# Performance work log

Measured on AMD Instinct MI355X. Metric: run time of the kernel, lower is better.

The kernel has to match this reference:

```python
import jax, jax.numpy as jnp
import numpy as np

N = 100000      # nodes
E = 1600000     # edges (avg degree 16)
IN_DIM = 64
OUT_DIM = 128
BN_EPS = 1e-5


def setup_inputs() -> dict:
    key = jax.random.key(0)
    kx, ke, kw, kb, ks = jax.random.split(key, 5)
    x = jax.random.normal(kx, (N, IN_DIM), dtype=jnp.float32)
    edge_index = jax.random.randint(ke, (2, E), 0, N, dtype=jnp.int32)
    # GCNConv linear weight (no bias inside lin; conv bias separate)
    W = jax.random.normal(kw, (IN_DIM, OUT_DIM), dtype=jnp.float32) / np.sqrt(IN_DIM)
    bias = jax.random.normal(kb, (OUT_DIM,), dtype=jnp.float32) * 0.01
    # skip projection Linear(in_dim, out_dim, bias=False)
    skip_W = jax.random.normal(ks, (IN_DIM, OUT_DIM), dtype=jnp.float32) / np.sqrt(IN_DIM)
    # BatchNorm1d affine params (training-mode batch stats used in forward)
    gamma = jnp.ones((OUT_DIM,), dtype=jnp.float32)
    beta = jnp.zeros((OUT_DIM,), dtype=jnp.float32)
    return {"x": x, "edge_index": edge_index, "W": W, "bias": bias,
            "skip_W": skip_W, "gamma": gamma, "beta": beta}


def _gcn_forward(x, edge_index, W, bias, skip_W, gamma, beta):
    n = x.shape[0]
    # GCNConv, normalize=True, add_self_loops=True (PyG defaults)
    row, col = edge_index[0], edge_index[1]
    loop = jnp.arange(n, dtype=edge_index.dtype)
    row_f = jnp.concatenate([row, loop])   # source nodes
    col_f = jnp.concatenate([col, loop])   # target nodes

    xt = x @ W                             # [N, OUT]
    deg = jax.ops.segment_sum(jnp.ones_like(col_f, dtype=xt.dtype), col_f,
                              num_segments=n)          # >= 1 due to self loops
    dinv = jax.lax.rsqrt(deg)
    norm = dinv[row_f] * dinv[col_f]                    # [E+N]
    msgs = xt[row_f] * norm[:, None]                    # gather + scale
    out = jax.ops.segment_sum(msgs, col_f, num_segments=n) + bias

    # skip-sum (in_dim != out_dim -> project)
    out = out + x @ skip_W

    # BatchNorm1d (training-mode batch statistics), affine
    mean = out.mean(axis=0)
    var = out.var(axis=0)
    out = (out - mean) * jax.lax.rsqrt(var + BN_EPS) * gamma + beta

    # ReLU; dropout p=0.0 -> identity
    return jax.nn.relu(out)


def reference(x, edge_index, W, bias, skip_W, gamma, beta):
    return _gcn_forward(x, edge_index, W, bias, skip_W, gamma, beta)
```

## Files before the change

### kernel.cpp

```cpp
#include <hip/hip_runtime.h>


typedef unsigned short ushort;
typedef __bf16 bf16x8 __attribute__((ext_vector_type(8)));
typedef float f32x4 __attribute__((ext_vector_type(4)));

constexpr int N_NODES = 100000;
constexpr int N_PAD   = 100096;
constexpr int E_EDGES = 1600000;

constexpr int BUCK_SHIFT = 7;
constexpr int NBUCK   = (N_NODES + 127) / 128;
constexpr int NBUCK_P = 784;
constexpr int CHUNK   = 4096;
constexpr int NCHUNK  = (E_EDGES + CHUNK - 1) / CHUNK;
constexpr int SORT_CAP = 4096;

constexpr size_t OFF_SCALE  = 0;
constexpr size_t OFF_DINV   = 256;
constexpr size_t OFF_ROWPTR = 100352;
constexpr size_t OFF_BASE   = 200480;
constexpr size_t OFF_GHIST  = 201280;
constexpr size_t OFF_PART   = OFF_GHIST;
constexpr size_t OFF_BINNED = 507824;
constexpr size_t OFF_XB     = 2107824;
constexpr size_t OFF_U      = 5310896;
constexpr size_t OFF_PRE    = 8513968;
constexpr size_t OFF_XD     = OFF_PRE;
constexpr size_t OFF_BT     = 14920112;

static __device__ __forceinline__ ushort f2bf(float f) {
    union { float f; unsigned u; } v; v.f = f;
    unsigned r = v.u + 0x7FFFu + ((v.u >> 16) & 1u);
    return (ushort)(r >> 16);
}
static __device__ __forceinline__ float bf2f(ushort u) {
    union { unsigned u; float f; } v; v.u = (unsigned)u << 16;
    return v.f;
}

__global__ void k_prep(const float* __restrict__ W, const float* __restrict__ skipW,
                       ushort* __restrict__ Bt) {
    int t = blockIdx.x * 256 + threadIdx.x;
    if (t >= 128 * 128) return;
    int k = t >> 7, n = t & 127;
    float v = (k < 64) ? W[k * 128 + n] : skipW[(k - 64) * 128 + n];
    Bt[n * 128 + k] = f2bf(v);
}

__global__ __launch_bounds__(256) void k_hist(const int* __restrict__ col,
                                              int* __restrict__ gh) {
    __shared__ int h[NBUCK_P];
    int c = blockIdx.x, t = threadIdx.x;
    for (int b = t; b < NBUCK_P; b += 256) h[b] = 0;
    __syncthreads();
    int e0 = c * CHUNK;
#pragma unroll
    for (int i = 0; i < CHUNK / 256; ++i) {
        int e = e0 + i * 256 + t;
        if (e < E_EDGES) atomicAdd(&h[col[e] >> BUCK_SHIFT], 1);
    }
    __syncthreads();
    for (int b = t; b < NBUCK_P; b += 256) gh[c * NBUCK_P + b] = h[b];
}

__global__ __launch_bounds__(512) void k_scan_buckets(int* __restrict__ gh,
                                                      int* __restrict__ base) {
    __shared__ int lds[512];
    int b = blockIdx.x, t = threadIdx.x;
    int v = (t < NCHUNK) ? gh[t * NBUCK_P + b] : 0;
    lds[t] = v;
    __syncthreads();
    int val = v;
#pragma unroll
    for (int off = 1; off < 512; off <<= 1) {
        int add = (t >= off) ? lds[t - off] : 0;
        __syncthreads();
        val += add;
        lds[t] = val;
        __syncthreads();
    }
    if (t < NCHUNK) gh[t * NBUCK_P + b] = val - v;
    if (t == 511) base[b] = val;
}

__global__ __launch_bounds__(1024) void k_scan_bases(int* __restrict__ base,
                                                     int* __restrict__ rowptr) {
    __shared__ int lds[1024];
    int t = threadIdx.x;
    int v = (t < NBUCK) ? base[t] : 0;
    lds[t] = v;
    __syncthreads();
    int val = v;
#pragma unroll
    for (int off = 1; off < 1024; off <<= 1) {
        int add = (t >= off) ? lds[t - off] : 0;
        __syncthreads();
        val += add;
        lds[t] = val;
        __syncthreads();
    }
    if (t < NBUCK) base[t] = val - v;
    if (t == 1023) {
        base[NBUCK] = val;
        rowptr[N_NODES] = val;
    }
}

__global__ __launch_bounds__(256) void k_scatter_bin(const int* __restrict__ row,
                                                     const int* __restrict__ col,
                                                     const int* __restrict__ gh,
                                                     const int* __restrict__ base,
                                                     unsigned int* __restrict__ binned) {
    __shared__ int cur[NBUCK_P];
    int c = blockIdx.x, t = threadIdx.x;
    for (int b = t; b < NBUCK_P; b += 256) {
        int bb = (b < NBUCK) ? base[b] : 0;
        cur[b] = bb + gh[c * NBUCK_P + b];
    }
    __syncthreads();
    int e0 = c * CHUNK;
#pragma unroll
    for (int i = 0; i < CHUNK / 256; ++i) {
        int e = e0 + i * 256 + t;
        if (e < E_EDGES) {
            int d = col[e];
            int s = row[e];
            int p = atomicAdd(&cur[d >> BUCK_SHIFT], 1);
            binned[p] = ((unsigned int)(d & 127) << 17) | (unsigned int)s;
        }
    }
}

__global__ __launch_bounds__(256) void k_sortbucket(unsigned int* __restrict__ binned,
                                                    const int* __restrict__ base,
                                                    int* __restrict__ rowptr,
                                                    float* __restrict__ dinv) {
    __shared__ unsigned int ebuf[SORT_CAP];
    __shared__ int sbuf[SORT_CAP];
    __shared__ int lcnt[128];
    __shared__ int scanb[128];
    __shared__ int lptr[128];
    int b = blockIdx.x, t = threadIdx.x;
    int i0 = base[b], i1 = base[b + 1];
    int cnt = i1 - i0;
    if (cnt > SORT_CAP) cnt = SORT_CAP;
    int n0 = b << BUCK_SHIFT;
    int nn = min(128, N_NODES - n0);

    for (int k = t; k < cnt; k += 256) ebuf[k] = binned[i0 + k];
    if (t < 128) lcnt[t] = 0;
    __syncthreads();
    for (int k = t; k < cnt; k += 256) atomicAdd(&lcnt[ebuf[k] >> 17], 1);
    __syncthreads();

    int myc = (t < 128) ? lcnt[t] : 0;
    if (t < 128) scanb[t] = myc;
    __syncthreads();
    int val = myc;
#pragma unroll
    for (int off = 1; off < 128; off <<= 1) {
        int add = (t < 128 && t >= off) ? scanb[t - off] : 0;
        __syncthreads();
        if (t < 128) {
            val += add;
            scanb[t] = val;
        }
        __syncthreads();
    }
    if (t < 128) {
        int excl = val - myc;
        lptr[t] = excl;
        if (t < nn) {
            rowptr[n0 + t] = i0 + excl;
            dinv[n0 + t] = rsqrtf((float)myc + 1.0f);
        }
    }
    __syncthreads();
    for (int k = t; k < cnt; k += 256) {
        unsigned int e = ebuf[k];
        int j = (int)(e >> 17);
        int p = atomicAdd(&lptr[j], 1);
        sbuf[p] = (int)(e & 0x1FFFF);
    }
    __syncthreads();
    for (int k = t; k < cnt; k += 256) binned[i0 + k] = (unsigned int)sbuf[k];
}

__global__ void k_cast_scale(const float* __restrict__ x, const float* __restrict__ dinv,
                             ushort* __restrict__ xb, ushort* __restrict__ xd) {
    int t = blockIdx.x * blockDim.x + threadIdx.x;
    if (t >= N_PAD * 16) return;
    int c = t >> 4;
    ushort4 b = {0, 0, 0, 0};
    ushort4 o = {0, 0, 0, 0};
    if (c < N_NODES) {
        float d = dinv[c];
        float4 v = ((const float4*)x)[t];
        b.x = f2bf(v.x); b.y = f2bf(v.y); b.z = f2bf(v.z); b.w = f2bf(v.w);
        o.x = f2bf(v.x * d); o.y = f2bf(v.y * d);
        o.z = f2bf(v.z * d); o.w = f2bf(v.w * d);
    }
    ((ushort4*)xb)[t] = b;
    ((ushort4*)xd)[t] = o;
}

__global__ __launch_bounds__(256) void k_agg(const ushort* __restrict__ xd,
                                             const float* __restrict__ dinv,
                                             const int* __restrict__ rowptr,
                                             const unsigned int* __restrict__ csr,
                                             ushort* __restrict__ u) {
    int t = blockIdx.x * blockDim.x + threadIdx.x;
    if (t >= N_PAD * 16) return;
    int c = t >> 4;
    int q = t & 15;
    if (c >= N_NODES) {
        ushort4 z = {0, 0, 0, 0};
        ((ushort4*)u)[t] = z;
        return;
    }
    float dc = dinv[c];
    ushort4 xv = ((const ushort4*)xd)[t];
    float4 acc;
    acc.x = bf2f(xv.x); acc.y = bf2f(xv.y);
    acc.z = bf2f(xv.z); acc.w = bf2f(xv.w);
    int i0 = rowptr[c], i1 = rowptr[c + 1];
    int i = i0;
    for (; i + 4 <= i1; i += 4) {
        int s0 = (int)csr[i];
        int s1 = (int)csr[i + 1];
        int s2 = (int)csr[i + 2];
        int s3 = (int)csr[i + 3];
        ushort4 v0 = ((const ushort4*)xd)[s0 * 16 + q];
        ushort4 v1 = ((const ushort4*)xd)[s1 * 16 + q];
        ushort4 v2 = ((const ushort4*)xd)[s2 * 16 + q];
        ushort4 v3 = ((const ushort4*)xd)[s3 * 16 + q];
        acc.x += bf2f(v0.x) + bf2f(v1.x) + bf2f(v2.x) + bf2f(v3.x);
        acc.y += bf2f(v0.y) + bf2f(v1.y) + bf2f(v2.y) + bf2f(v3.y);
        acc.z += bf2f(v0.z) + bf2f(v1.z) + bf2f(v2.z) + bf2f(v3.z);
        acc.w += bf2f(v0.w) + bf2f(v1.w) + bf2f(v2.w) + bf2f(v3.w);
    }
    for (; i < i1; ++i) {
        int s = (int)csr[i];
        ushort4 v = ((const ushort4*)xd)[s * 16 + q];
        acc.x += bf2f(v.x); acc.y += bf2f(v.y);
        acc.z += bf2f(v.z); acc.w += bf2f(v.w);
    }
    ushort4 o;
    o.x = f2bf(acc.x * dc); o.y = f2bf(acc.y * dc);
    o.z = f2bf(acc.z * dc); o.w = f2bf(acc.w * dc);
    ((ushort4*)u)[t] = o;
}

__global__ __launch_bounds__(256) void k_gemm(const ushort* __restrict__ u,
                                              const ushort* __restrict__ xb,
                                              const ushort* __restrict__ Bt,
                                              const float* __restrict__ bias,
                                              ushort* __restrict__ pre,
                                              float* __restrict__ partial) {
    __shared__ float sred[128];
    __shared__ float qred[128];
    int tid = threadIdx.x;
    int wave = tid >> 6, lane = tid & 63;
    int wm = wave >> 1, wn = wave & 1;
    int l15 = lane & 15, quad = lane >> 4;
    int row0 = blockIdx.x * 128 + wm * 64;
    int col0 = wn * 64;

    if (tid < 128) { sred[tid] = 0.f; qred[tid] = 0.f; }
    __syncthreads();

    bf16x8 af[4][4], bf_[4][4];
#pragma unroll
    for (int kc = 0; kc < 4; ++kc) {
        const ushort* abase = (kc < 2) ? u : xb;
        int ko = (kc & 1) * 32 + quad * 8;
#pragma unroll
        for (int im = 0; im < 4; ++im)
            af[kc][im] = *(const bf16x8*)&abase[(size_t)(row0 + im * 16 + l15) * 64 + ko];
#pragma unroll
        for (int jn = 0; jn < 4; ++jn)
            bf_[kc][jn] = *(const bf16x8*)&Bt[(size_t)(col0 + jn * 16 + l15) * 128 + kc * 32 + quad * 8];
    }

    f32x4 acc[4][4];
#pragma unroll
    for (int a = 0; a < 4; ++a)
#pragma unroll
        for (int b = 0; b < 4; ++b) acc[a][b] = (f32x4){0.f, 0.f, 0.f, 0.f};

#pragma unroll
    for (int kc = 0; kc < 4; ++kc)
#pragma unroll
        for (int im = 0; im < 4; ++im)
#pragma unroll
            for (int jn = 0; jn < 4; ++jn)
                acc[im][jn] = __builtin_amdgcn_mfma_f32_16x16x32_bf16(
                    af[kc][im], bf_[kc][jn], acc[im][jn], 0, 0, 0);

    int coln[4];
    float bi[4];
#pragma unroll
    for (int jn = 0; jn < 4; ++jn) {
        coln[jn] = col0 + jn * 16 + l15;
        bi[jn] = bias[coln[jn]];
    }
    float lsum[4] = {0.f, 0.f, 0.f, 0.f};
    float lsq[4]  = {0.f, 0.f, 0.f, 0.f};
#pragma unroll
    for (int im = 0; im < 4; ++im) {
        int rbase = row0 + im * 16 + quad * 4;
#pragma unroll
        for (int r = 0; r < 4; ++r) {
            int rowi = rbase + r;
            if (rowi < N_NODES) {
#pragma unroll
                for (int jn = 0; jn < 4; ++jn) {
                    float v = acc[im][jn][r] + bi[jn];
                    pre[(size_t)rowi * 128 + coln[jn]] = f2bf(v);
                    lsum[jn] += v;
                    lsq[jn]  += v * v;
                }
            }
        }
    }
#pragma unroll
    for (int jn = 0; jn < 4; ++jn) {
        atomicAdd(&sred[coln[jn]], lsum[jn]);
        atomicAdd(&qred[coln[jn]], lsq[jn]);
    }
    __syncthreads();
    if (tid < 128) {
        partial[(size_t)blockIdx.x * 256 + tid]       = sred[tid];
        partial[(size_t)blockIdx.x * 256 + 128 + tid] = qred[tid];
    }
}

__global__ __launch_bounds__(256) void k_reduce(const float* __restrict__ partial,
                                                const float* __restrict__ gamma,
                                                const float* __restrict__ beta,
                                                float* __restrict__ scaleshift) {
    __shared__ float ls[256], lq[256];
    int j = blockIdx.x;
    int t = threadIdx.x;
    float s = 0.f, q = 0.f;
    for (int p = t; p < NBUCK; p += 256) {
        s += partial[(size_t)p * 256 + j];
        q += partial[(size_t)p * 256 + 128 + j];
    }
    ls[t] = s; lq[t] = q;
    __syncthreads();
#pragma unroll
    for (int off = 128; off > 0; off >>= 1) {
        if (t < off) { ls[t] += ls[t + off]; lq[t] += lq[t + off]; }
        __syncthreads();
    }
    if (t == 0) {
        float mean = ls[0] * (1.0f / N_NODES);
        float var  = lq[0] * (1.0f / N_NODES) - mean * mean;
        float sc   = gamma[j] * rsqrtf(var + 1e-5f);
        scaleshift[j]       = sc;
        scaleshift[128 + j] = beta[j] - mean * sc;
    }
}

__global__ void k_apply(const ushort* __restrict__ pre, float* __restrict__ out,
                        const float* __restrict__ scaleshift) {
    int t = blockIdx.x * blockDim.x + threadIdx.x;
    if (t >= N_NODES * 32) return;
    int j4 = t & 31;
    ushort4 p = ((const ushort4*)pre)[t];
    float4 sc = ((const float4*)scaleshift)[j4];
    float4 sh = ((const float4*)(scaleshift + 128))[j4];
    float4 v;
    v.x = fmaxf(fmaf(bf2f(p.x), sc.x, sh.x), 0.f);
    v.y = fmaxf(fmaf(bf2f(p.y), sc.y, sh.y), 0.f);
    v.z = fmaxf(fmaf(bf2f(p.z), sc.z, sh.z), 0.f);
    v.w = fmaxf(fmaf(bf2f(p.w), sc.w, sh.w), 0.f);
    ((float4*)out)[t] = v;
}

extern "C" void kernel_launch(void* const* d_in, const int* in_sizes, int n_in,
                              void* d_out, int out_size, void* d_ws, size_t ws_size,
                              hipStream_t stream) {
    const float* x      = (const float*)d_in[0];
    const int*   eidx   = (const int*)d_in[1];
    const float* W      = (const float*)d_in[2];
    const float* bias   = (const float*)d_in[3];
    const float* skipW  = (const float*)d_in[4];
    const float* gamma  = (const float*)d_in[5];
    const float* beta   = (const float*)d_in[6];
    float* out = (float*)d_out;
    float* ws  = (float*)d_ws;

    const int* row = eidx;
    const int* col = eidx + E_EDGES;

    float* scaleshift = ws + OFF_SCALE;
    float* dinv       = ws + OFF_DINV;
    int*   rowptr     = (int*)(ws + OFF_ROWPTR);
    int*   base       = (int*)(ws + OFF_BASE);
    int*   gh         = (int*)(ws + OFF_GHIST);
    float* partial    = ws + OFF_PART;
    unsigned int* binned = (unsigned int*)(ws + OFF_BINNED);
    ushort* xb        = (ushort*)(ws + OFF_XB);
    ushort* u         = (ushort*)(ws + OFF_U);
    ushort* xd        = (ushort*)(ws + OFF_XD);
    ushort* pre       = (ushort*)(ws + OFF_PRE);
    ushort* Bt        = (ushort*)(ws + OFF_BT);

    k_prep<<<64, 256, 0, stream>>>(W, skipW, Bt);
    k_hist<<<NCHUNK, 256, 0, stream>>>(col, gh);
    k_scan_buckets<<<NBUCK, 512, 0, stream>>>(gh, base);
    k_scan_bases<<<1, 1024, 0, stream>>>(base, rowptr);
    k_scatter_bin<<<NCHUNK, 256, 0, stream>>>(row, col, gh, base, binned);
    k_sortbucket<<<NBUCK, 256, 0, stream>>>(binned, base, rowptr, dinv);
    k_cast_scale<<<(N_PAD * 16 + 255) / 256, 256, 0, stream>>>(x, dinv, xb, xd);
    k_agg<<<(N_PAD * 16 + 255) / 256, 256, 0, stream>>>(xd, dinv, rowptr, binned, u);
    k_gemm<<<NBUCK, 256, 0, stream>>>(u, xb, Bt, bias, pre, partial);
    k_reduce<<<128, 256, 0, stream>>>(partial, gamma, beta, scaleshift);
    k_apply<<<(N_NODES * 32 + 255) / 256, 256, 0, stream>>>(pre, out, scaleshift);
}
```

Measured before the change: 241.8 us.

## Store scaled features as FP8, fuse cast into sort kernel, unroll gather by 8

The degree-scaled feature copy used by the aggregation gather is now stored as FP8 (4 bytes per 4 features) instead of bf16, halving gather traffic. The separate cast/scale kernel is folded into the per-bucket sort kernel, using its shared dinv values, which removes a launch and one pass over x. The aggregation loop is unrolled to 8 neighbors for more loads in flight. FP8 quantization of messages lowers accuracy and may break tolerance.

```diff
diff --git a/kernel.cpp b/kernel.cpp
--- a/kernel.cpp
+++ b/kernel.cpp
@@ -4,6 +4,7 @@
 typedef unsigned short ushort;
 typedef __bf16 bf16x8 __attribute__((ext_vector_type(8)));
 typedef float f32x4 __attribute__((ext_vector_type(4)));
+typedef float f32x2 __attribute__((ext_vector_type(2)));
 
 constexpr int N_NODES = 100000;
 constexpr int N_PAD   = 100096;
@@ -26,7 +27,7 @@
 constexpr size_t OFF_XB     = 2107824;
 constexpr size_t OFF_U      = 5310896;
 constexpr size_t OFF_PRE    = 8513968;
-constexpr size_t OFF_XD     = OFF_PRE;
+constexpr size_t OFF_XD8    = OFF_PRE;
 constexpr size_t OFF_BT     = 14920112;
 
 static __device__ __forceinline__ ushort f2bf(float f) {
@@ -37,6 +38,12 @@
 static __device__ __forceinline__ float bf2f(ushort u) {
     union { unsigned u; float f; } v; v.u = (unsigned)u << 16;
     return v.f;
+}
+static __device__ __forceinline__ unsigned pack_fp8x4(float a, float b, float c, float d) {
+    int r = 0;
+    r = __builtin_amdgcn_cvt_pk_fp8_f32(a, b, r, false);
+    r = __builtin_amdgcn_cvt_pk_fp8_f32(c, d, r, true);
+    return (unsigned)r;
 }
 
 __global__ void k_prep(const float* __restrict__ W, const float* __restrict__ skipW,
@@ -135,12 +142,16 @@
 __global__ __launch_bounds__(256) void k_sortbucket(unsigned int* __restrict__ binned,
                                                     const int* __restrict__ base,
                                                     int* __restrict__ rowptr,
-                                                    float* __restrict__ dinv) {
+                                                    float* __restrict__ dinv,
+                                                    const float* __restrict__ x,
+                                                    ushort* __restrict__ xb,
+                                                    unsigned* __restrict__ xd8) {
     __shared__ unsigned int ebuf[SORT_CAP];
     __shared__ int sbuf[SORT_CAP];
     __shared__ int lcnt[128];
     __shared__ int scanb[128];
     __shared__ int lptr[128];
+    __shared__ float ldinv[128];
     int b = blockIdx.x, t = threadIdx.x;
     int i0 = base[b], i1 = base[b + 1];
     int cnt = i1 - i0;
@@ -171,9 +182,11 @@
     if (t < 128) {
         int excl = val - myc;
         lptr[t] = excl;
+        float dv = rsqrtf((float)myc + 1.0f);
+        ldinv[t] = dv;
         if (t < nn) {
             rowptr[n0 + t] = i0 + excl;
-            dinv[n0 + t] = rsqrtf((float)myc + 1.0f);
+            dinv[n0 + t] = dv;
         }
     }
     __syncthreads();
@@ -185,27 +198,26 @@
     }
     __syncthreads();
     for (int k = t; k < cnt; k += 256) binned[i0 + k] = (unsigned int)sbuf[k];
-}
-
-__global__ void k_cast_scale(const float* __restrict__ x, const float* __restrict__ dinv,
-                             ushort* __restrict__ xb, ushort* __restrict__ xd) {
-    int t = blockIdx.x * blockDim.x + threadIdx.x;
-    if (t >= N_PAD * 16) return;
-    int c = t >> 4;
-    ushort4 b = {0, 0, 0, 0};
-    ushort4 o = {0, 0, 0, 0};
-    if (c < N_NODES) {
-        float d = dinv[c];
-        float4 v = ((const float4*)x)[t];
-        b.x = f2bf(v.x); b.y = f2bf(v.y); b.z = f2bf(v.z); b.w = f2bf(v.w);
-        o.x = f2bf(v.x * d); o.y = f2bf(v.y * d);
-        o.z = f2bf(v.z * d); o.w = f2bf(v.w * d);
-    }
-    ((ushort4*)xb)[t] = b;
-    ((ushort4*)xd)[t] = o;
-}
-
-__global__ __launch_bounds__(256) void k_agg(const ushort* __restrict__ xd,
+
+#pragma unroll
+    for (int it = 0; it < 8; ++it) {
+        int idx = it * 256 + t;
+        int nl = idx >> 4, q = idx & 15;
+        int c = n0 + nl;
+        ushort4 bb = {0, 0, 0, 0};
+        unsigned w8 = 0;
+        if (nl < nn) {
+            float4 v = ((const float4*)x)[(size_t)c * 16 + q];
+            bb.x = f2bf(v.x); bb.y = f2bf(v.y); bb.z = f2bf(v.z); bb.w = f2bf(v.w);
+            float d = ldinv[nl];
+            w8 = pack_fp8x4(v.x * d, v.y * d, v.z * d, v.w * d);
+        }
+        ((ushort4*)xb)[(size_t)c * 16 + q] = bb;
+        xd8[(size_t)c * 16 + q] = w8;
+    }
+}
+
+__global__ __launch_bounds__(256) void k_agg(const unsigned* __restrict__ xd8,
                                              const float* __restrict__ dinv,
                                              const int* __restrict__ rowptr,
                                              const unsigned int* __restrict__ csr,
@@ -220,31 +232,34 @@
         return;
     }
     float dc = dinv[c];
-    ushort4 xv = ((const ushort4*)xd)[t];
     float4 acc;
-    acc.x = bf2f(xv.x); acc.y = bf2f(xv.y);
-    acc.z = bf2f(xv.z); acc.w = bf2f(xv.w);
+    {
+        unsigned w = xd8[t];
+        f32x2 lo = __builtin_amdgcn_cvt_pk_f32_fp8((int)w, false);
+        f32x2 hi = __builtin_amdgcn_cvt_pk_f32_fp8((int)w, true);
+        acc.x = lo.x; acc.y = lo.y; acc.z = hi.x; acc.w = hi.y;
+    }
     int i0 = rowptr[c], i1 = rowptr[c + 1];
     int i = i0;
-    for (; i + 4 <= i1; i += 4) {
-        int s0 = (int)csr[i];
-        int s1 = (int)csr[i + 1];
-        int s2 = (int)csr[i + 2];
-        int s3 = (int)csr[i + 3];
-        ushort4 v0 = ((const ushort4*)xd)[s0 * 16 + q];
-        ushort4 v1 = ((const ushort4*)xd)[s1 * 16 + q];
-        ushort4 v2 = ((const ushort4*)xd)[s2 * 16 + q];
-        ushort4 v3 = ((const ushort4*)xd)[s3 * 16 + q];
-        acc.x += bf2f(v0.x) + bf2f(v1.x) + bf2f(v2.x) + bf2f(v3.x);
-        acc.y += bf2f(v0.y) + bf2f(v1.y) + bf2f(v2.y) + bf2f(v3.y);
-        acc.z += bf2f(v0.z) + bf2f(v1.z) + bf2f(v2.z) + bf2f(v3.z);
-        acc.w += bf2f(v0.w) + bf2f(v1.w) + bf2f(v2.w) + bf2f(v3.w);
+    for (; i + 8 <= i1; i += 8) {
+        int s[8];
+#pragma unroll
+        for (int k = 0; k < 8; ++k) s[k] = (int)csr[i + k];
+        unsigned w[8];
+#pragma unroll
+        for (int k = 0; k < 8; ++k) w[k] = xd8[s[k] * 16 + q];
+#pragma unroll
+        for (int k = 0; k < 8; ++k) {
+            f32x2 lo = __builtin_amdgcn_cvt_pk_f32_fp8((int)w[k], false);
+            f32x2 hi = __builtin_amdgcn_cvt_pk_f32_fp8((int)w[k], true);
+            acc.x += lo.x; acc.y += lo.y; acc.z += hi.x; acc.w += hi.y;
+        }
     }
     for (; i < i1; ++i) {
-        int s = (int)csr[i];
-        ushort4 v = ((const ushort4*)xd)[s * 16 + q];
-        acc.x += bf2f(v.x); acc.y += bf2f(v.y);
-        acc.z += bf2f(v.z); acc.w += bf2f(v.w);
+        unsigned w = xd8[(int)csr[i] * 16 + q];
+        f32x2 lo = __builtin_amdgcn_cvt_pk_f32_fp8((int)w, false);
+        f32x2 hi = __builtin_amdgcn_cvt_pk_f32_fp8((int)w, true);
+        acc.x += lo.x; acc.y += lo.y; acc.z += hi.x; acc.w += hi.y;
     }
     ushort4 o;
     o.x = f2bf(acc.x * dc); o.y = f2bf(acc.y * dc);
@@ -405,7 +420,7 @@
     unsigned int* binned = (unsigned int*)(ws + OFF_BINNED);
     ushort* xb        = (ushort*)(ws + OFF_XB);
     ushort* u         = (ushort*)(ws + OFF_U);
-    ushort* xd        = (ushort*)(ws + OFF_XD);
+    unsigned* xd8     = (unsigned*)(ws + OFF_XD8);
     ushort* pre       = (ushort*)(ws + OFF_PRE);
     ushort* Bt        = (ushort*)(ws + OFF_BT);
 
@@ -414,9 +429,8 @@
     k_scan_buckets<<<NBUCK, 512, 0, stream>>>(gh, base);
     k_scan_bases<<<1, 1024, 0, stream>>>(base, rowptr);
     k_scatter_bin<<<NCHUNK, 256, 0, stream>>>(row, col, gh, base, binned);
-    k_sortbucket<<<NBUCK, 256, 0, stream>>>(binned, base, rowptr, dinv);
-    k_cast_scale<<<(N_PAD * 16 + 255) / 256, 256, 0, stream>>>(x, dinv, xb, xd);
-    k_agg<<<(N_PAD * 16 + 255) / 256, 256, 0, stream>>>(xd, dinv, rowptr, binned, u);
+    k_sortbucket<<<NBUCK, 256, 0, stream>>>(binned, base, rowptr, dinv, x, xb, xd8);
+    k_agg<<<(N_PAD * 16 + 255) / 256, 256, 0, stream>>>(xd8, dinv, rowptr, binned, u);
     k_gemm<<<NBUCK, 256, 0, stream>>>(u, xb, Bt, bias, pre, partial);
     k_reduce<<<128, 256, 0, stream>>>(partial, gamma, beta, scaleshift);
     k_apply<<<(N_NODES * 32 + 255) / 256, 256, 0, stream>>>(pre, out, scaleshift);
```

After: 230.0 us. 4.8% less time.
